# Performance work log

Measured on AMD Instinct MI355X. Metric: run time of the kernel, lower is better.

## Reference

```python
import math
import jax, jax.numpy as jnp
import numpy as np

RANK = 8
OUT_H, OUT_W = 512, 512
CTX = 512
EPS = 1e-12          # module eps (fp32 path)
NORM_EPS = 1e-12     # torch F.normalize default eps
REPULSION = 0.1
NOISE = 0.01
OUT_FEATS = 26 * RANK + 2  # 24r + 2r + 2


def _l2norm(x):
    n = jnp.sqrt(jnp.sum(x * x, axis=-1, keepdims=True))
    return x / jnp.maximum(n, NORM_EPS)


def _stable(x):
    # forward: clamp tiny magnitudes to +/-eps; backward: identity (straight-through)
    s = jnp.where(jnp.abs(x) < EPS, jnp.sign(x) * EPS, x)
    return x + jax.lax.stop_gradient(s - x)


def setup_inputs() -> dict:
    key = jax.random.key(0)
    k1, k2, k3, k4 = jax.random.split(key, 4)
    x = jax.random.normal(k1, (4, CTX), jnp.float32)
    # xavier_uniform for Linear(CTX -> OUT_FEATS)
    bound = math.sqrt(6.0 / (CTX + OUT_FEATS))
    ctx_w = jax.random.uniform(k2, (OUT_FEATS, CTX), jnp.float32, -bound, bound)
    ctx_b = jax.random.uniform(k3, (OUT_FEATS,), jnp.float32, -1.0, 1.0) / math.sqrt(CTX)
    weights = jax.random.normal(k4, (1, RANK, 2, 2, OUT_H, OUT_W, 2), jnp.float32) * 1e-5
    return {"x": x, "ctx_w": ctx_w, "ctx_b": ctx_b, "weights": weights}


def reference(x, ctx_w, ctx_b, weights):
    r = RANK
    B = x.shape[0]
    xt = x @ ctx_w.T + ctx_b                      # [B, 26r+2]
    sa = 13 * r + 1                               # slice_attention
    xt = xt[:, :sa] * jnp.tanh(xt[:, sa:])        # [B, 13r+1]
    mod = xt[:, : 12 * r].reshape(B, r, 3, 2, 1, 1, 2)  # [B,r,3,2,1,1,2]
    shift_lerp = jnp.array([0.5, 0.0], xt.dtype)
    shift_scale = jnp.array([1.0, 0.0], xt.dtype)
    c = mod[:, :, 0] + shift_lerp                 # [B,r,2,1,1,2]
    bias = mod[:, :, 1]
    scale = mod[:, :, 2] + shift_scale
    w0, w1 = weights[:, :, 0], weights[:, :, 1]   # [1,r,2,H,W,2]
    # complex lerp: z = w0 + c*(w1 - w0)
    dr = w1[..., 0] - w0[..., 0]
    di = w1[..., 1] - w0[..., 1]
    lr = w0[..., 0] + c[..., 0] * dr - c[..., 1] * di
    li = w0[..., 1] + c[..., 0] * di + c[..., 1] * dr
    # complex addmul: z = bias + z*scale
    zr = bias[..., 0] + lr * scale[..., 0] - li * scale[..., 1]
    zi = bias[..., 1] + lr * scale[..., 1] + li * scale[..., 0]
    z = jnp.stack([zr, zi], axis=-1)              # [B,r,2,H,W,2]
    num, den = z[:, :, 0], z[:, :, 1]             # [B,r,H,W,2]
    dnorm = jnp.sqrt(jnp.clip(jnp.sum(den * den, -1), EPS, None))[..., None]
    theta = den / dnorm
    w = jnp.sum(num * theta, -1)                  # [B,r,H,W]
    wf = w.reshape(B, r, -1)                      # [B,r,H*W]
    wf = _l2norm(_stable(wf))
    # self-similarity repulsion (small r x r matmuls)
    sim = jnp.einsum('brn,bsn->brs', wf, wf)
    sim = sim * (1.0 - jnp.eye(r, dtype=wf.dtype))
    rep = jnp.einsum('brs,bsn->brn', sim, wf) / (r - 1)
    wf = wf - rep * (REPULSION / math.sqrt(r))
    wf = _l2norm(_stable(wf))
    # deterministic noise injection (training mode with fixed key)
    mean = jax.lax.stop_gradient(jnp.mean(wf, -1, keepdims=True))
    std = jax.lax.stop_gradient(jnp.clip(jnp.std(wf, -1, keepdims=True, ddof=1), EPS, None))
    noise = jax.random.normal(jax.random.key(42), wf.shape, wf.dtype)
    wf = wf + jax.lax.stop_gradient((noise * std + mean) * NOISE)
    w = wf.reshape(B, r, OUT_H, OUT_W)
    w = jnp.concatenate([w, jnp.zeros((B, 1, OUT_H, OUT_W), w.dtype)], axis=1)  # drain
    wr = xt[:, 12 * r:]                           # [B, r+1]
    wr = jnp.concatenate([wr[:, :-1], wr[:, -1:] + 1.0 / math.sqrt(r)], axis=-1)
    wr = jax.nn.softmax(_l2norm(wr), axis=-1)
    return jnp.sum(w * wr[:, :, None, None], axis=1)  # [B,H,W]
```

## Files before the change

kernel.cpp:

```cpp
#include <hip/hip_runtime.h>
#include <hip/hip_fp16.h>
#include <math.h>

#define NPIX 262144
#define BATCH 4
#define RANK 8
#define CTXD 512
#define OUTF 210

#define XT_OFF   0
#define ACC_OFF  1024
#define REP      8
#define NACC     176
#define WFS_OFF  4096

__device__ __forceinline__ float dpp_sum64(float x) {
  x += __int_as_float(__builtin_amdgcn_update_dpp(0, __float_as_int(x), 0x111, 0xf, 0xf, true));
  x += __int_as_float(__builtin_amdgcn_update_dpp(0, __float_as_int(x), 0x112, 0xf, 0xf, true));
  x += __int_as_float(__builtin_amdgcn_update_dpp(0, __float_as_int(x), 0x114, 0xf, 0xf, true));
  x += __int_as_float(__builtin_amdgcn_update_dpp(0, __float_as_int(x), 0x118, 0xf, 0xf, true));
  x += __int_as_float(__builtin_amdgcn_update_dpp(0, __float_as_int(x), 0x142, 0xf, 0xf, true));
  x += __int_as_float(__builtin_amdgcn_update_dpp(0, __float_as_int(x), 0x143, 0xf, 0xf, true));
  return x;
}

__device__ __forceinline__ void threefry2x32_pair(unsigned int x0, unsigned int x1,
                                                  unsigned int* o0, unsigned int* o1) {
  const unsigned int ks0 = 0u, ks1 = 42u, ks2 = 0x1BD11BF0u;
  x0 += ks0; x1 += ks1;
#define TF_R(rot) { x0 += x1; x1 = (x1 << rot) | (x1 >> (32 - rot)); x1 ^= x0; }
  TF_R(13) TF_R(15) TF_R(26) TF_R(6)
  x0 += ks1; x1 += ks2 + 1u;
  TF_R(17) TF_R(29) TF_R(16) TF_R(24)
  x0 += ks2; x1 += ks0 + 2u;
  TF_R(13) TF_R(15) TF_R(26) TF_R(6)
  x0 += ks0; x1 += ks1 + 3u;
  TF_R(17) TF_R(29) TF_R(16) TF_R(24)
  x0 += ks1; x1 += ks2 + 4u;
  TF_R(13) TF_R(15) TF_R(26) TF_R(6)
  x0 += ks2; x1 += ks0 + 5u;
#undef TF_R
  *o0 = x0; *o1 = x1;
}

__device__ __forceinline__ float fast_normal(unsigned int bits) {
  unsigned int fb = (bits >> 9) | 0x3f800000u;
  float f = __uint_as_float(fb) - 1.0f;
  const float lo = -0.99999994039535522461f;
  float u = f * 2.0f + lo;
  u = fmaxf(u, lo);
  float w = -__logf(fmaf(-u, u, 1.0f));
  float q1 = w - 2.5f;
  float p1 = 0.00021858087f;
  p1 = fmaf(p1, q1, -0.00125372503f);
  p1 = fmaf(p1, q1, -0.00417768164f);
  p1 = fmaf(p1, q1, 0.246640727f);
  p1 = fmaf(p1, q1, 1.50140941f);
  float q2 = sqrtf(w) - 3.0f;
  float p2 = 0.00573950773f;
  p2 = fmaf(p2, q2, -0.0076224613f);
  p2 = fmaf(p2, q2, 0.00943887047f);
  p2 = fmaf(p2, q2, 1.00167406f);
  p2 = fmaf(p2, q2, 2.83297682f);
  float pr = (w < 5.0f) ? p1 : p2;
  return 1.4142135623730951f * pr * u;
}

__global__ __launch_bounds__(256) void k_ctx(const float* __restrict__ x,
                                             const float* __restrict__ cw,
                                             const float* __restrict__ cb,
                                             float* __restrict__ ws) {
  int gi = blockIdx.x * 256 + threadIdx.x;
  if (gi < REP * NACC) ws[ACC_OFF + gi] = 0.f;

  int lane = threadIdx.x & 63, wv = threadIdx.x >> 6;
  int row = blockIdx.x * 4 + wv;
  int b = row / OUTF, i = row - b * OUTF;
  const float* wrow = cw + i * CTXD;
  const float* xr = x + b * CTXD;
  float acc = 0.f;
#pragma unroll
  for (int u = 0; u < CTXD; u += 64)
    acc = fmaf(wrow[u + lane], xr[u + lane], acc);
  acc = dpp_sum64(acc);
  if (lane == 63) ws[XT_OFF + row] = acc + cb[i];
}

__global__ __launch_bounds__(128) void k_wfs(const float* __restrict__ wts,
                                             float* __restrict__ ws) {
  __shared__ float4 mods[32][3];
  __shared__ float gred[2][NACC];
  const float* xt = ws + XT_OFF;
  __half2* wfs2 = (__half2*)((char*)ws + WFS_OFF * 4);
  int t = threadIdx.x;

  if (t < 96) {
    int bk = t / 3, part = t - bk * 3;
    int b = bk >> 3, k = bk & 7;
    const float* xb = xt + b * OUTF + 12 * k;
#define GATE(j) (xb[j] * tanhf(xb[105 + (j)]))
    float4 r;
    if (part < 2) {
      float c0 = GATE(2 * part) + 0.5f;
      float c1 = GATE(2 * part + 1);
      float s0 = GATE(8 + 2 * part) + 1.0f;
      float s1 = GATE(9 + 2 * part);
      float omc = 1.0f - c0;
      r.x = s0 * omc + s1 * c1;
      r.y = s1 * omc - s0 * c1;
      r.z = s0 * c0 - s1 * c1;
      r.w = s1 * c0 + s0 * c1;
    } else {
      r.x = GATE(4); r.y = GATE(5); r.z = GATE(6); r.w = GATE(7);
    }
#undef GATE
    mods[bk][part] = r;
  }
  __syncthreads();

  int tp = blockIdx.x * 128 + t;
  const float4* w4 = (const float4*)wts;
  float wf[BATCH][RANK][2];
#pragma unroll
  for (int k = 0; k < RANK; ++k) {
    float4 ld[2][2];
#pragma unroll
    for (int s = 0; s < 2; ++s)
#pragma unroll
      for (int comp = 0; comp < 2; ++comp)
        ld[s][comp] = w4[((k * 4 + s * 2 + comp) << 17) + tp];
#pragma unroll
    for (int b = 0; b < BATCH; ++b) {
      float4 P  = mods[b * 8 + k][0];
      float4 Q  = mods[b * 8 + k][1];
      float4 Bb = mods[b * 8 + k][2];
      __half2 st;
#pragma unroll
      for (int j = 0; j < 2; ++j) {
        float w0r = j ? ld[0][0].z : ld[0][0].x;
        float w0i = j ? ld[0][0].w : ld[0][0].y;
        float w1r = j ? ld[1][0].z : ld[1][0].x;
        float w1i = j ? ld[1][0].w : ld[1][0].y;
        float v0r = j ? ld[0][1].z : ld[0][1].x;
        float v0i = j ? ld[0][1].w : ld[0][1].y;
        float v1r = j ? ld[1][1].z : ld[1][1].x;
        float v1i = j ? ld[1][1].w : ld[1][1].y;
        float zr0 = fmaf(P.x, w0r, fmaf(-P.y, w0i, fmaf(P.z, w1r, fmaf(-P.w, w1i, Bb.x))));
        float zi0 = fmaf(P.y, w0r, fmaf( P.x, w0i, fmaf(P.w, w1r, fmaf( P.z, w1i, Bb.y))));
        float zr1 = fmaf(Q.x, v0r, fmaf(-Q.y, v0i, fmaf(Q.z, v1r, fmaf(-Q.w, v1i, Bb.z))));
        float zi1 = fmaf(Q.y, v0r, fmaf( Q.x, v0i, fmaf(Q.w, v1r, fmaf( Q.z, v1i, Bb.w))));
        float d2 = fmaxf(fmaf(zr1, zr1, zi1 * zi1), 1e-12f);
        float rn = __builtin_amdgcn_rsqf(d2);
        float w = fmaf(zr0, zr1, zi0 * zi1) * rn;
        wf[b][k][j] = w;
        if (j) st.y = __float2half(w); else st.x = __float2half(w);
      }
      wfs2[((b * RANK + k) << 17) + tp] = st;
    }
  }
  int lane = t & 63, wv = t >> 6;
#pragma unroll
  for (int b = 0; b < BATCH; ++b) {
    int idx = b * 36;
#pragma unroll
    for (int r = 0; r < RANK; ++r)
#pragma unroll
      for (int s = r; s < RANK; ++s, ++idx) {
        float pr = dpp_sum64(fmaf(wf[b][r][0], wf[b][s][0], wf[b][r][1] * wf[b][s][1]));
        if (lane == 63) gred[wv][idx] = pr;
      }
  }
#pragma unroll
  for (int b = 0; b < BATCH; ++b)
#pragma unroll
    for (int k = 0; k < RANK; ++k) {
      float pr = dpp_sum64(wf[b][k][0] + wf[b][k][1]);
      if (lane == 63) gred[wv][144 + b * 8 + k] = pr;
    }
  __syncthreads();
  for (int i = t; i < NACC; i += 128) {
    float s = gred[0][i] + gred[1][i];
    atomicAdd(ws + ACC_OFF + (blockIdx.x & (REP - 1)) * NACC + i, s);
  }
}

__global__ __launch_bounds__(256) void k_out(const float* __restrict__ ws,
                                             float* __restrict__ out) {
  const float* xt = ws + XT_OFF;
  const __half* wfs16 = (const __half*)((const char*)ws + WFS_OFF * 4);
  __shared__ float G[NACC];
  __shared__ float n1[32], Ml[256], vv[32], scl[32], ca[4], wrl[BATCH][9];
  __shared__ float in2[32], mnv[32], sdv[32];
  int t = threadIdx.x;
  if (t < NACC) {
    float s = 0.f;
#pragma unroll
    for (int rep = 0; rep < REP; ++rep) s += ws[ACC_OFF + rep * NACC + t];
    G[t] = s;
  }
  if (t >= 192 && t < 192 + BATCH) {
    int b = t - 192;
    float raw[9];
#pragma unroll
    for (int j = 0; j < 9; ++j)
      raw[j] = xt[b * OUTF + 96 + j] * tanhf(xt[b * OUTF + 201 + j]);
    raw[8] += 0.35355339059327373f;
    double ss = 0.0;
    for (int j = 0; j < 9; ++j) ss += (double)raw[j] * (double)raw[j];
    float n = fmaxf((float)sqrt(ss), 1e-12f);
    float y[9]; float m = -1e30f;
    for (int j = 0; j < 9; ++j) { y[j] = raw[j] / n; m = fmaxf(m, y[j]); }
    float e[9]; double se = 0.0;
    for (int j = 0; j < 9; ++j) { e[j] = expf(y[j] - m); se += (double)e[j]; }
    for (int j = 0; j < 9; ++j) wrl[b][j] = e[j] / (float)se;
  }
  __syncthreads();
  if (t < 32) {
    int b = t >> 3, k = t & 7;
    int di = k * 8 - (k * (k - 1)) / 2;
    n1[t] = fmaxf(sqrtf(G[b * 36 + di]), 1e-12f);
  }
  __syncthreads();
  {
    int b = t >> 6, k = (t >> 3) & 7, s = t & 7;
    float m;
    if (k == s) {
      m = 1.0f / n1[b * 8 + k];
    } else {
      int r0 = k < s ? k : s, s0 = k < s ? s : k;
      int gi = r0 * 8 - (r0 * (r0 - 1)) / 2 + (s0 - r0);
      float simv = G[b * 36 + gi] / (n1[b * 8 + k] * n1[b * 8 + s]);
      m = -0.0050507627227610544f * simv / n1[b * 8 + s];
    }
    Ml[t] = m;
  }
  __syncthreads();
  if (t < 32) {
    int b = t >> 3, k = t & 7;
    float sum = 0.f, sq = 0.f;
#pragma unroll
    for (int s = 0; s < 8; ++s) {
      float ms = Ml[b * 64 + k * 8 + s];
      sum = fmaf(ms, G[144 + b * 8 + s], sum);
#pragma unroll
      for (int u = 0; u < 8; ++u) {
        int r0 = s < u ? s : u, s0 = s < u ? u : s;
        int gi = r0 * 8 - (r0 * (r0 - 1)) / 2 + (s0 - r0);
        sq = fmaf(ms * Ml[b * 64 + k * 8 + u], G[b * 36 + gi], sq);
      }
    }
    float n2 = fmaxf(sqrtf(fmaxf(sq, 0.f)), 1e-12f);
    float mean = sum / n2 * (1.0f / NPIX);
    float sy2 = sq / (n2 * n2);
    float var = (sy2 - (float)NPIX * mean * mean) * (1.0f / (float)(NPIX - 1));
    var = fmaxf(var, 0.f);
    float sd = fmaxf(sqrtf(var), 1e-12f);
    in2[t] = 1.f / n2; mnv[t] = mean; sdv[t] = sd;
  }
  __syncthreads();
  if (t < 32) {
    int b = t >> 3, s = t & 7;
    float acc = 0.f;
#pragma unroll
    for (int k = 0; k < 8; ++k)
      acc += wrl[b][k] * Ml[b * 64 + k * 8 + s] * in2[b * 8 + k];
    vv[t] = acc;
    scl[t] = wrl[b][s] * 0.01f * sdv[t];
  }
  if (t < BATCH) {
    float a = 0.f;
#pragma unroll
    for (int k = 0; k < 8; ++k) a += wrl[t][k] * 0.01f * mnv[t * 8 + k];
    ca[t] = a;
  }
  __syncthreads();

  int p = blockIdx.x * 256 + t;
  float o[4];
#pragma unroll
  for (int b = 0; b < 4; ++b) {
    float acc = ca[b];
#pragma unroll
    for (int s = 0; s < 8; ++s)
      acc = fmaf(vv[b * 8 + s], __half2float(wfs16[((b * RANK + s) << 18) + p]), acc);
    o[b] = acc;
  }
#pragma unroll
  for (int bk = 0; bk < 16; ++bk) {
    unsigned int i = ((unsigned int)bk << 18) + (unsigned int)p;
    unsigned int r0, r1;
    threefry2x32_pair(i, i + 0x400000u, &r0, &r1);
    int b2 = bk >> 3, k = bk & 7;
    o[b2]     += scl[b2 * 8 + k]       * fast_normal(r0);
    o[b2 + 2] += scl[(b2 + 2) * 8 + k] * fast_normal(r1);
  }
#pragma unroll
  for (int b = 0; b < 4; ++b) out[(b << 18) + p] = o[b];
}

extern "C" void kernel_launch(void* const* d_in, const int* in_sizes, int n_in,
                              void* d_out, int out_size, void* d_ws, size_t ws_size,
                              hipStream_t stream) {
  const float* x   = (const float*)d_in[0];
  const float* cw  = (const float*)d_in[1];
  const float* cb  = (const float*)d_in[2];
  const float* wts = (const float*)d_in[3];
  float* out = (float*)d_out;
  float* ws  = (float*)d_ws;

  k_ctx <<<210,  256, 0, stream>>>(x, cw, cb, ws);
  k_wfs <<<1024, 128, 0, stream>>>(wts, ws);
  k_out <<<1024, 256, 0, stream>>>(ws, out);
}
```

Baseline: 137.5 us.

## Fuse wfs and output kernels with a grid barrier, keeping wf in registers

Merges the per-pixel wf computation and the output pass into one persistent kernel of 512 blocks. A software grid barrier (an atomic counter plus spin) waits until the global Gram/sum reductions are complete. The fp16 round-trip of wf through the workspace is removed because wf stays in registers, and the noise generation is moved before the barrier so it overlaps with the reduction wait. The cost is higher register pressure (wf plus noise kept live) and the requirement that all 512 blocks be co-resident, otherwise the barrier deadlocks.

Result: slower. 301.1 us (+119.0%).

```diff
diff --git a/kernel.cpp b/kernel.cpp
--- a/kernel.cpp
+++ b/kernel.cpp
@@ -9,10 +9,11 @@
 #define OUTF 210
 
 #define XT_OFF   0
+#define BAR_IDX  1016
 #define ACC_OFF  1024
 #define REP      8
 #define NACC     176
-#define WFS_OFF  4096
+#define NBLK     512
 
 __device__ __forceinline__ float dpp_sum64(float x) {
   x += __int_as_float(__builtin_amdgcn_update_dpp(0, __float_as_int(x), 0x111, 0xf, 0xf, true));
@@ -72,6 +73,7 @@
                                              float* __restrict__ ws) {
   int gi = blockIdx.x * 256 + threadIdx.x;
   if (gi < REP * NACC) ws[ACC_OFF + gi] = 0.f;
+  if (gi == 0) ((unsigned int*)ws)[BAR_IDX] = 0u;
 
   int lane = threadIdx.x & 63, wv = threadIdx.x >> 6;
   int row = blockIdx.x * 4 + wv;
@@ -86,12 +88,16 @@
   if (lane == 63) ws[XT_OFF + row] = acc + cb[i];
 }
 
-__global__ __launch_bounds__(128) void k_wfs(const float* __restrict__ wts,
-                                             float* __restrict__ ws) {
+__global__ __launch_bounds__(256, 2) void k_fused(const float* __restrict__ wts,
+                                                  float* __restrict__ ws,
+                                                  float* __restrict__ out) {
   __shared__ float4 mods[32][3];
-  __shared__ float gred[2][NACC];
+  __shared__ float gred[4][NACC];
+  __shared__ float G[NACC];
+  __shared__ float n1[32], Ml[256], vv[32], scl[32], ca[4], wrl[BATCH][9];
+  __shared__ float in2[32], mnv[32], sdv[32];
+
   const float* xt = ws + XT_OFF;
-  __half2* wfs2 = (__half2*)((char*)ws + WFS_OFF * 4);
   int t = threadIdx.x;
 
   if (t < 96) {
@@ -118,9 +124,10 @@
   }
   __syncthreads();
 
-  int tp = blockIdx.x * 128 + t;
+  int tp = blockIdx.x * 256 + t;
   const float4* w4 = (const float4*)wts;
   float wf[BATCH][RANK][2];
+  __half2 nzA[16], nzB[16];
 #pragma unroll
   for (int k = 0; k < RANK; ++k) {
     float4 ld[2][2];
@@ -129,12 +136,23 @@
 #pragma unroll
       for (int comp = 0; comp < 2; ++comp)
         ld[s][comp] = w4[((k * 4 + s * 2 + comp) << 17) + tp];
+
+#pragma unroll
+    for (int b2 = 0; b2 < 2; ++b2) {
+      int bk = b2 * 8 + k;
+      unsigned int i0 = ((unsigned int)bk << 18) + 2u * (unsigned int)tp;
+      unsigned int ra0, ra1, rb0, rb1;
+      threefry2x32_pair(i0,      i0 + 0x400000u, &ra0, &ra1);
+      threefry2x32_pair(i0 + 1u, i0 + 0x400001u, &rb0, &rb1);
+      nzA[bk] = __halves2half2(__float2half(fast_normal(ra0)), __float2half(fast_normal(rb0)));
+      nzB[bk] = __halves2half2(__float2half(fast_normal(ra1)), __float2half(fast_normal(rb1)));
+    }
+
 #pragma unroll
     for (int b = 0; b < BATCH; ++b) {
       float4 P  = mods[b * 8 + k][0];
       float4 Q  = mods[b * 8 + k][1];
       float4 Bb = mods[b * 8 + k][2];
-      __half2 st;
 #pragma unroll
       for (int j = 0; j < 2; ++j) {
         float w0r = j ? ld[0][0].z : ld[0][0].x;
@@ -151,13 +169,11 @@
         float zi1 = fmaf(Q.y, v0r, fmaf( Q.x, v0i, fmaf(Q.w, v1r, fmaf( Q.z, v1i, Bb.w))));
         float d2 = fmaxf(fmaf(zr1, zr1, zi1 * zi1), 1e-12f);
         float rn = __builtin_amdgcn_rsqf(d2);
-        float w = fmaf(zr0, zr1, zi0 * zi1) * rn;
-        wf[b][k][j] = w;
-        if (j) st.y = __float2half(w); else st.x = __float2half(w);
+        wf[b][k][j] = fmaf(zr0, zr1, zi0 * zi1) * rn;
       }
-      wfs2[((b * RANK + k) << 17) + tp] = st;
-    }
-  }
+    }
+  }
+
   int lane = t & 63, wv = t >> 6;
 #pragma unroll
   for (int b = 0; b < BATCH; ++b) {
@@ -165,8 +181,8 @@
 #pragma unroll
     for (int r = 0; r < RANK; ++r)
 #pragma unroll
-      for (int s = r; s < RANK; ++s, ++idx) {
-        float pr = dpp_sum64(fmaf(wf[b][r][0], wf[b][s][0], wf[b][r][1] * wf[b][s][1]));
+      for (int s2 = r; s2 < RANK; ++s2, ++idx) {
+        float pr = dpp_sum64(fmaf(wf[b][r][0], wf[b][s2][0], wf[b][r][1] * wf[b][s2][1]));
         if (lane == 63) gred[wv][idx] = pr;
       }
   }
@@ -178,24 +194,26 @@
       if (lane == 63) gred[wv][144 + b * 8 + k] = pr;
     }
   __syncthreads();
-  for (int i = t; i < NACC; i += 128) {
-    float s = gred[0][i] + gred[1][i];
+  for (int i = t; i < NACC; i += 256) {
+    float s = gred[0][i] + gred[1][i] + gred[2][i] + gred[3][i];
     atomicAdd(ws + ACC_OFF + (blockIdx.x & (REP - 1)) * NACC + i, s);
   }
-}
-
-__global__ __launch_bounds__(256) void k_out(const float* __restrict__ ws,
-                                             float* __restrict__ out) {
-  const float* xt = ws + XT_OFF;
-  const __half* wfs16 = (const __half*)((const char*)ws + WFS_OFF * 4);
-  __shared__ float G[NACC];
-  __shared__ float n1[32], Ml[256], vv[32], scl[32], ca[4], wrl[BATCH][9];
-  __shared__ float in2[32], mnv[32], sdv[32];
-  int t = threadIdx.x;
+
+  __syncthreads();
+  if (t == 0) {
+    unsigned int* bar = (unsigned int*)ws + BAR_IDX;
+    __hip_atomic_fetch_add(bar, 1u, __ATOMIC_ACQ_REL, __HIP_MEMORY_SCOPE_AGENT);
+    while (__hip_atomic_load(bar, __ATOMIC_ACQUIRE, __HIP_MEMORY_SCOPE_AGENT) < (unsigned int)NBLK)
+      __builtin_amdgcn_s_sleep(1);
+  }
+  __syncthreads();
+
   if (t < NACC) {
     float s = 0.f;
 #pragma unroll
-    for (int rep = 0; rep < REP; ++rep) s += ws[ACC_OFF + rep * NACC + t];
+    for (int rep = 0; rep < REP; ++rep)
+      s += __hip_atomic_load(ws + ACC_OFF + rep * NACC + t,
+                             __ATOMIC_RELAXED, __HIP_MEMORY_SCOPE_AGENT);
     G[t] = s;
   }
   if (t >= 192 && t < 192 + BATCH) {
@@ -275,27 +293,30 @@
   }
   __syncthreads();
 
-  int p = blockIdx.x * 256 + t;
-  float o[4];
-#pragma unroll
-  for (int b = 0; b < 4; ++b) {
-    float acc = ca[b];
-#pragma unroll
-    for (int s = 0; s < 8; ++s)
-      acc = fmaf(vv[b * 8 + s], __half2float(wfs16[((b * RANK + s) << 18) + p]), acc);
-    o[b] = acc;
-  }
-#pragma unroll
-  for (int bk = 0; bk < 16; ++bk) {
-    unsigned int i = ((unsigned int)bk << 18) + (unsigned int)p;
-    unsigned int r0, r1;
-    threefry2x32_pair(i, i + 0x400000u, &r0, &r1);
-    int b2 = bk >> 3, k = bk & 7;
-    o[b2]     += scl[b2 * 8 + k]       * fast_normal(r0);
-    o[b2 + 2] += scl[(b2 + 2) * 8 + k] * fast_normal(r1);
-  }
-#pragma unroll
-  for (int b = 0; b < 4; ++b) out[(b << 18) + p] = o[b];
+  float o0[4], o1[4];
+#pragma unroll
+  for (int b = 0; b < 4; ++b) { o0[b] = ca[b]; o1[b] = ca[b]; }
+#pragma unroll
+  for (int b = 0; b < 4; ++b)
+#pragma unroll
+    for (int s = 0; s < 8; ++s) {
+      float v = vv[b * 8 + s];
+      o0[b] = fmaf(v, wf[b][s][0], o0[b]);
+      o1[b] = fmaf(v, wf[b][s][1], o1[b]);
+    }
+#pragma unroll
+  for (int b2 = 0; b2 < 2; ++b2)
+#pragma unroll
+    for (int k = 0; k < 8; ++k) {
+      int bk = b2 * 8 + k;
+      o0[b2]     = fmaf(scl[b2 * 8 + k],       __low2float (nzA[bk]), o0[b2]);
+      o1[b2]     = fmaf(scl[b2 * 8 + k],       __high2float(nzA[bk]), o1[b2]);
+      o0[b2 + 2] = fmaf(scl[(b2 + 2) * 8 + k], __low2float (nzB[bk]), o0[b2 + 2]);
+      o1[b2 + 2] = fmaf(scl[(b2 + 2) * 8 + k], __high2float(nzB[bk]), o1[b2 + 2]);
+    }
+#pragma unroll
+  for (int b = 0; b < 4; ++b)
+    ((float2*)out)[(b << 17) + tp] = make_float2(o0[b], o1[b]);
 }
 
 extern "C" void kernel_launch(void* const* d_in, const int* in_sizes, int n_in,
@@ -308,7 +329,6 @@
   float* out = (float*)d_out;
   float* ws  = (float*)d_ws;
 
-  k_ctx <<<210,  256, 0, stream>>>(x, cw, cb, ws);
-  k_wfs <<<1024, 128, 0, stream>>>(wts, ws);
-  k_out <<<1024, 256, 0, stream>>>(ws, out);
-}
+  k_ctx  <<<210,  256, 0, stream>>>(x, cw, cb, ws);
+  k_fused<<<NBLK, 256, 0, stream>>>(wts, ws, out);
+}
```
